# Kernel tuning notes

Hardware: AMD Instinct MI355X
Metric: run time of the kernel (lower is better)

Reference implementation:

```python
import jax, jax.numpy as jnp
import numpy as np


def gcn_conv(x, src, dst, deg_inv_sqrt, W, b):
    # PyG GCNConv: h = x @ W, then symmetric-normalized scatter-add over edges
    # (edge list already includes self-loops; deg computed over it).
    h = x @ W                                   # [N, F_out]
    norm = deg_inv_sqrt[src] * deg_inv_sqrt[dst]  # [E]
    msgs = h[src] * norm[:, None]               # gather + scale
    out = jax.ops.segment_sum(msgs, dst, num_segments=x.shape[0])
    return out + b


def setup_inputs() -> dict:
    key = jax.random.key(0)
    k1, k2, k3, k4 = jax.random.split(key, 4)
    N, E, F_in, F_hid, F_out = 200000, 6400000, 128, 8, 16
    x = jax.random.normal(k1, (N, F_in), dtype=jnp.float32)
    edge_index = jax.random.randint(k2, (2, E), 0, N, dtype=jnp.int64)
    W1 = jax.random.normal(k3, (F_in, F_hid), dtype=jnp.float32) * (1.0 / np.sqrt(F_in))
    b1 = jnp.zeros((F_hid,), dtype=jnp.float32)
    W2 = jax.random.normal(k4, (F_hid, F_out), dtype=jnp.float32) * (1.0 / np.sqrt(F_hid))
    b2 = jnp.zeros((F_out,), dtype=jnp.float32)
    return {"x": x, "edge_index": edge_index, "W1": W1, "b1": b1, "W2": W2, "b2": b2}


def reference(x, edge_index, W1, b1, W2, b2):
    N = x.shape[0]
    # add self-loops (GCNConv default add_self_loops=True)
    loops = jnp.arange(N, dtype=edge_index.dtype)
    src = jnp.concatenate([edge_index[0], loops])
    dst = jnp.concatenate([edge_index[1], loops])
    deg = jax.ops.segment_sum(jnp.ones_like(dst, dtype=x.dtype), dst, num_segments=N)
    deg_inv_sqrt = jnp.where(deg > 0, jax.lax.rsqrt(deg), 0.0)
    h = jax.nn.relu(gcn_conv(x, src, dst, deg_inv_sqrt, W1, b1))
    # dropout is identity in eval mode (training=False)
    out = gcn_conv(h, src, dst, deg_inv_sqrt, W2, b2)
    return out
```

## Files before the change

### kernel.cpp

```cpp
#include <hip/hip_runtime.h>
#include <hip/hip_fp16.h>

#define F_IN  128
#define F_HID 8
#define F_OUT 16

#define SBSH  9
#define SBW   (1 << SBSH)
#define MAXB  400
#define BIN_CAP  32
#define FLUSH_G  16


__global__ void init_gcur(int* __restrict__ gcur, int cap, int B) {
    int b = blockIdx.x * blockDim.x + threadIdx.x;
    if (b < B) gcur[b] = b * cap;
}

__global__ __launch_bounds__(512) void stage_bin(const int* __restrict__ ei,
                                                 int* __restrict__ gcur,
                                                 int* __restrict__ stage,
                                                 int E, int B, int per_block) {
    __shared__ int bin_cnt[MAXB];
    __shared__ int bin_buf[MAXB * BIN_CAP];
    for (int i = threadIdx.x; i < B; i += blockDim.x) bin_cnt[i] = 0;
    __syncthreads();
    const bool vec = ((E & 3) == 0);
    int base = blockIdx.x * per_block;
    int end  = min(E, base + per_block);
    for (int it = base; it < end; it += (int)blockDim.x * 4) {
        int e = it + (int)threadIdx.x * 4;
        int sv[4], dv[4], m4 = 0;
        if (vec && e + 3 < end) {
            int4 s4 = *(const int4*)(ei + e);
            int4 d4 = *(const int4*)(ei + E + e);
            sv[0] = s4.x; sv[1] = s4.y; sv[2] = s4.z; sv[3] = s4.w;
            dv[0] = d4.x; dv[1] = d4.y; dv[2] = d4.z; dv[3] = d4.w;
            m4 = 4;
        } else {
            for (int q = 0; e + q < end && q < 4; q++) { sv[q] = ei[e + q]; dv[q] = ei[E + e + q]; m4++; }
        }
        for (int q = 0; q < m4; q++) {
            int b   = dv[q] >> SBSH;
            int val = (sv[q] << SBSH) | (dv[q] & (SBW - 1));
            int pos = atomicAdd(&bin_cnt[b], 1);
            if (pos < BIN_CAP) {
                bin_buf[b * BIN_CAP + ((pos + b) & (BIN_CAP - 1))] = val;
            } else {
                int gp = atomicAdd(&gcur[b], 1);
                stage[gp] = val;
            }
        }
        __syncthreads();
        for (int b2 = threadIdx.x; b2 < B; b2 += blockDim.x) {
            int c = min(bin_cnt[b2], BIN_CAP);
            if (c >= FLUSH_G) {
                int m = c & ~(FLUSH_G - 1);
                int r = atomicAdd(&gcur[b2], m);
                for (int k = 0; k < m; k++)
                    stage[r + k] = bin_buf[b2 * BIN_CAP + ((k + b2) & (BIN_CAP - 1))];
                for (int k = m; k < c; k++)
                    bin_buf[b2 * BIN_CAP + ((k - m + b2) & (BIN_CAP - 1))] =
                        bin_buf[b2 * BIN_CAP + ((k + b2) & (BIN_CAP - 1))];
                bin_cnt[b2] = c - m;
            } else {
                bin_cnt[b2] = c;
            }
        }
        __syncthreads();
    }
    for (int b2 = threadIdx.x; b2 < B; b2 += blockDim.x) {
        int c = min(bin_cnt[b2], BIN_CAP);
        if (c > 0) {
            int r = atomicAdd(&gcur[b2], c);
            for (int k = 0; k < c; k++)
                stage[r + k] = bin_buf[b2 * BIN_CAP + ((k + b2) & (BIN_CAP - 1))];
        }
    }
}

__global__ __launch_bounds__(512) void scatter_csr(const int* __restrict__ stage,
                                                   const int* __restrict__ gcur,
                                                   int cap,
                                                   int* __restrict__ cnt,
                                                   float* __restrict__ dis,
                                                   int* __restrict__ row_start,
                                                   int* __restrict__ csr, int n) {
    __shared__ int s0[SBW], s1[SBW];
    int b  = blockIdx.x;
    int nb = b << SBSH;
    int i  = threadIdx.x;
    s0[i] = 0;
    __syncthreads();
    int base = b * cap;
    int num  = gcur[b] - base;
    for (int k = i; k < num; k += 512)
        atomicAdd(&s0[stage[base + k] & (SBW - 1)], 1);
    __syncthreads();
    int c = s0[i];
    if (nb + i < n) { cnt[nb + i] = c; dis[nb + i] = rsqrtf((float)(c + 1)); }
    int* src = s0; int* dst = s1;
    for (int off = 1; off < SBW; off <<= 1) {
        int v = src[i] + ((i >= off) ? src[i - off] : 0);
        dst[i] = v;
        __syncthreads();
        int* t = src; src = dst; dst = t;
    }
    int e = base + src[i] - c;
    if (nb + i < n) row_start[nb + i] = e;
    dst[i] = e;
    __syncthreads();
    for (int k = i; k < num; k += 512) {
        int v = stage[base + k];
        int pos = atomicAdd(&dst[v & (SBW - 1)], 1);
        csr[pos] = v >> SBSH;
    }
}

__global__ __launch_bounds__(256) void gemm1(const float* __restrict__ x,
                                             const float* __restrict__ W1,
                                             const float* __restrict__ dis,
                                             __half* __restrict__ g1, int n) {
    __shared__ float w[F_IN * F_HID];
    for (int i = threadIdx.x; i < F_IN * F_HID; i += blockDim.x) w[i] = W1[i];
    __syncthreads();
    int node = blockIdx.x * blockDim.x + threadIdx.x;
    if (node >= n) return;
    const float4* xr = (const float4*)(x + (size_t)node * F_IN);
    float acc[F_HID];
#pragma unroll
    for (int f = 0; f < F_HID; f++) acc[f] = 0.0f;
#pragma unroll
    for (int j = 0; j < F_IN / 4; j++) {
        float4 v = xr[j];
        const float* wr = &w[j * 4 * F_HID];
#pragma unroll
        for (int f = 0; f < F_HID; f++)
            acc[f] += v.x * wr[f] + v.y * wr[F_HID + f] + v.z * wr[2 * F_HID + f] + v.w * wr[3 * F_HID + f];
    }
    float d = dis[node];
    __half2 h[4];
#pragma unroll
    for (int p = 0; p < 4; p++) h[p] = __floats2half2_rn(acc[2 * p] * d, acc[2 * p + 1] * d);
    *(uint4*)(g1 + (size_t)node * F_HID) = *(uint4*)h;
}

__global__ __launch_bounds__(256) void aggregate_relu(const int* __restrict__ csr,
                                                      const int* __restrict__ row_start,
                                                      const int* __restrict__ cnt,
                                                      const float* __restrict__ dis,
                                                      const float* __restrict__ b1,
                                                      const __half* __restrict__ gin,
                                                      __half* __restrict__ gout, int n) {
    __shared__ float bb[F_HID];
    if (threadIdx.x < F_HID) bb[threadIdx.x] = b1[threadIdx.x];
    __syncthreads();
    int t = blockIdx.x * blockDim.x + threadIdx.x;
    int node = t >> 3;
    int f = t & 7;
    if (node >= n) return;
    int beg = row_start[node];
    int c   = cnt[node];
    float acc = __half2float(gin[(size_t)node * F_HID + f]);
    int j = 0;
    for (; j + 3 < c; j += 4) {
        int s0 = __builtin_nontemporal_load(csr + beg + j);
        int s1 = __builtin_nontemporal_load(csr + beg + j + 1);
        int s2 = __builtin_nontemporal_load(csr + beg + j + 2);
        int s3 = __builtin_nontemporal_load(csr + beg + j + 3);
        float a0 = __half2float(gin[(size_t)s0 * F_HID + f]);
        float a1 = __half2float(gin[(size_t)s1 * F_HID + f]);
        float a2 = __half2float(gin[(size_t)s2 * F_HID + f]);
        float a3 = __half2float(gin[(size_t)s3 * F_HID + f]);
        acc += (a0 + a1) + (a2 + a3);
    }
    for (; j < c; j++) {
        int s = __builtin_nontemporal_load(csr + beg + j);
        acc += __half2float(gin[(size_t)s * F_HID + f]);
    }
    float d = dis[node];
    float r = fmaxf(acc * d + bb[f], 0.0f) * d;
    gout[(size_t)node * F_HID + f] = __float2half(r);
}

__global__ __launch_bounds__(256) void aggregate_out(const int* __restrict__ csr,
                                                     const int* __restrict__ row_start,
                                                     const int* __restrict__ cnt,
                                                     const float* __restrict__ dis,
                                                     const float* __restrict__ W2,
                                                     const float* __restrict__ b2,
                                                     const __half* __restrict__ gin,
                                                     float* __restrict__ out, int n) {
    __shared__ float w[F_HID * F_OUT];
    __shared__ float bb[F_OUT];
    if (threadIdx.x < F_HID * F_OUT) w[threadIdx.x] = W2[threadIdx.x];
    if (threadIdx.x < F_OUT) bb[threadIdx.x] = b2[threadIdx.x];
    __syncthreads();
    int t = blockIdx.x * blockDim.x + threadIdx.x;
    int node = t >> 3;
    int f = t & 7;
    if (node >= n) return;
    int beg = row_start[node];
    int c   = cnt[node];
    float acc = __half2float(gin[(size_t)node * F_HID + f]);
    int j = 0;
    for (; j + 3 < c; j += 4) {
        int s0 = __builtin_nontemporal_load(csr + beg + j);
        int s1 = __builtin_nontemporal_load(csr + beg + j + 1);
        int s2 = __builtin_nontemporal_load(csr + beg + j + 2);
        int s3 = __builtin_nontemporal_load(csr + beg + j + 3);
        float a0 = __half2float(gin[(size_t)s0 * F_HID + f]);
        float a1 = __half2float(gin[(size_t)s1 * F_HID + f]);
        float a2 = __half2float(gin[(size_t)s2 * F_HID + f]);
        float a3 = __half2float(gin[(size_t)s3 * F_HID + f]);
        acc += (a0 + a1) + (a2 + a3);
    }
    for (; j < c; j++) {
        int s = __builtin_nontemporal_load(csr + beg + j);
        acc += __half2float(gin[(size_t)s * F_HID + f]);
    }
    float a_self = acc * dis[node];
    float o0 = bb[2 * f], o1 = bb[2 * f + 1];
#pragma unroll
    for (int k = 0; k < 8; k++) {
        float ak = __shfl(a_self, k, 8);
        o0 += ak * w[k * F_OUT + 2 * f];
        o1 += ak * w[k * F_OUT + 2 * f + 1];
    }
    *(float2*)(out + (size_t)node * F_OUT + 2 * f) = make_float2(o0, o1);
}

extern "C" void kernel_launch(void* const* d_in, const int* in_sizes, int n_in,
                              void* d_out, int out_size, void* d_ws, size_t ws_size,
                              hipStream_t stream) {
    const float* x  = (const float*)d_in[0];
    const int*   ei = (const int*)d_in[1];
    const float* W1 = (const float*)d_in[2];
    const float* b1 = (const float*)d_in[3];
    const float* W2 = (const float*)d_in[4];
    const float* b2 = (const float*)d_in[5];
    float* out = (float*)d_out;

    const int N = in_sizes[0] / F_IN;
    const int E = in_sizes[1] / 2;
    const int B = (N + SBW - 1) >> SBSH;

    int avg = (E + B - 1) / B;
    int cap = (avg + avg / 16 + 255) & ~255;

    int*    stage     = (int*)d_ws;
    int*    csr       = stage + (size_t)B * cap;
    float*  dis       = (float*)(csr + (size_t)B * cap);
    __half* gA        = (__half*)(dis + N);
    __half* gB        = (__half*)((int*)gA + (size_t)N * 4);
    int*    cnt       = (int*)gB + (size_t)N * 4;
    int*    row_start = cnt + N;
    int*    gcur      = row_start + N;

    const int BT = 256;
    dim3 blkN((N + BT - 1) / BT), thr(BT);
    dim3 blkA(((size_t)N * F_HID + BT - 1) / BT);

    int per_block = ((E + 639) / 640 + 2047) & ~2047;
    int SBLK = (E + per_block - 1) / per_block;

    init_gcur     <<<dim3((B + BT - 1) / BT), thr, 0, stream>>>(gcur, cap, B);
    stage_bin     <<<dim3(SBLK), dim3(512), 0, stream>>>(ei, gcur, stage, E, B, per_block);
    scatter_csr   <<<dim3(B),   dim3(512), 0, stream>>>(stage, gcur, cap, cnt, dis, row_start, csr, N);
    gemm1         <<<blkN, thr, 0, stream>>>(x, W1, dis, gA, N);
    aggregate_relu<<<blkA, thr, 0, stream>>>(csr, row_start, cnt, dis, b1, gA, gB, N);
    aggregate_out <<<blkA, thr, 0, stream>>>(csr, row_start, cnt, dis, W2, b2, gB, out, N);
}
```

Measured before the change: 464.6 us.

## Flush bins with whole wavefronts and aggregate features as half2 pairs

```diff
diff --git a/kernel.cpp b/kernel.cpp
--- a/kernel.cpp
+++ b/kernel.cpp
@@ -26,6 +26,8 @@
     for (int i = threadIdx.x; i < B; i += blockDim.x) bin_cnt[i] = 0;
     __syncthreads();
     const bool vec = ((E & 3) == 0);
+    const int wave = threadIdx.x >> 6;
+    const int lane = threadIdx.x & 63;
     int base = blockIdx.x * per_block;
     int end  = min(E, base + per_block);
     for (int it = base; it < end; it += (int)blockDim.x * 4) {
@@ -52,29 +54,34 @@
             }
         }
         __syncthreads();
-        for (int b2 = threadIdx.x; b2 < B; b2 += blockDim.x) {
+        for (int b2 = wave; b2 < B; b2 += 8) {
             int c = min(bin_cnt[b2], BIN_CAP);
             if (c >= FLUSH_G) {
                 int m = c & ~(FLUSH_G - 1);
-                int r = atomicAdd(&gcur[b2], m);
-                for (int k = 0; k < m; k++)
-                    stage[r + k] = bin_buf[b2 * BIN_CAP + ((k + b2) & (BIN_CAP - 1))];
-                for (int k = m; k < c; k++)
-                    bin_buf[b2 * BIN_CAP + ((k - m + b2) & (BIN_CAP - 1))] =
-                        bin_buf[b2 * BIN_CAP + ((k + b2) & (BIN_CAP - 1))];
-                bin_cnt[b2] = c - m;
-            } else {
+                int r = 0;
+                if (lane == 0) r = atomicAdd(&gcur[b2], m);
+                r = __shfl(r, 0);
+                if (lane < m)
+                    stage[r + lane] = bin_buf[b2 * BIN_CAP + ((lane + b2) & (BIN_CAP - 1))];
+                int rem = c - m;
+                int tmp = 0;
+                if (lane < rem) tmp = bin_buf[b2 * BIN_CAP + ((m + lane + b2) & (BIN_CAP - 1))];
+                if (lane < rem) bin_buf[b2 * BIN_CAP + ((lane + b2) & (BIN_CAP - 1))] = tmp;
+                if (lane == 0) bin_cnt[b2] = rem;
+            } else if (lane == 0) {
                 bin_cnt[b2] = c;
             }
         }
         __syncthreads();
     }
-    for (int b2 = threadIdx.x; b2 < B; b2 += blockDim.x) {
+    for (int b2 = wave; b2 < B; b2 += 8) {
         int c = min(bin_cnt[b2], BIN_CAP);
         if (c > 0) {
-            int r = atomicAdd(&gcur[b2], c);
-            for (int k = 0; k < c; k++)
-                stage[r + k] = bin_buf[b2 * BIN_CAP + ((k + b2) & (BIN_CAP - 1))];
+            int r = 0;
+            if (lane == 0) r = atomicAdd(&gcur[b2], c);
+            r = __shfl(r, 0);
+            if (lane < c)
+                stage[r + lane] = bin_buf[b2 * BIN_CAP + ((lane + b2) & (BIN_CAP - 1))];
         }
     }
 }
@@ -150,37 +157,40 @@
                                                       const int* __restrict__ cnt,
                                                       const float* __restrict__ dis,
                                                       const float* __restrict__ b1,
-                                                      const __half* __restrict__ gin,
-                                                      __half* __restrict__ gout, int n) {
+                                                      const __half2* __restrict__ gin,
+                                                      __half2* __restrict__ gout, int n) {
     __shared__ float bb[F_HID];
     if (threadIdx.x < F_HID) bb[threadIdx.x] = b1[threadIdx.x];
     __syncthreads();
     int t = blockIdx.x * blockDim.x + threadIdx.x;
-    int node = t >> 3;
-    int f = t & 7;
+    int node = t >> 2;
+    int f2 = t & 3;
     if (node >= n) return;
     int beg = row_start[node];
     int c   = cnt[node];
-    float acc = __half2float(gin[(size_t)node * F_HID + f]);
+    float2 acc = __half22float2(gin[(size_t)node * 4 + f2]);
     int j = 0;
     for (; j + 3 < c; j += 4) {
         int s0 = __builtin_nontemporal_load(csr + beg + j);
         int s1 = __builtin_nontemporal_load(csr + beg + j + 1);
         int s2 = __builtin_nontemporal_load(csr + beg + j + 2);
         int s3 = __builtin_nontemporal_load(csr + beg + j + 3);
-        float a0 = __half2float(gin[(size_t)s0 * F_HID + f]);
-        float a1 = __half2float(gin[(size_t)s1 * F_HID + f]);
-        float a2 = __half2float(gin[(size_t)s2 * F_HID + f]);
-        float a3 = __half2float(gin[(size_t)s3 * F_HID + f]);
-        acc += (a0 + a1) + (a2 + a3);
+        float2 a0 = __half22float2(gin[(size_t)s0 * 4 + f2]);
+        float2 a1 = __half22float2(gin[(size_t)s1 * 4 + f2]);
+        float2 a2 = __half22float2(gin[(size_t)s2 * 4 + f2]);
+        float2 a3 = __half22float2(gin[(size_t)s3 * 4 + f2]);
+        acc.x += (a0.x + a1.x) + (a2.x + a3.x);
+        acc.y += (a0.y + a1.y) + (a2.y + a3.y);
     }
     for (; j < c; j++) {
         int s = __builtin_nontemporal_load(csr + beg + j);
-        acc += __half2float(gin[(size_t)s * F_HID + f]);
+        float2 a = __half22float2(gin[(size_t)s * 4 + f2]);
+        acc.x += a.x; acc.y += a.y;
     }
     float d = dis[node];
-    float r = fmaxf(acc * d + bb[f], 0.0f) * d;
-    gout[(size_t)node * F_HID + f] = __float2half(r);
+    float r0 = fmaxf(acc.x * d + bb[2 * f2], 0.0f) * d;
+    float r1 = fmaxf(acc.y * d + bb[2 * f2 + 1], 0.0f) * d;
+    gout[(size_t)node * 4 + f2] = __floats2half2_rn(r0, r1);
 }
 
 __global__ __launch_bounds__(256) void aggregate_out(const int* __restrict__ csr,
@@ -189,7 +199,7 @@
                                                      const float* __restrict__ dis,
                                                      const float* __restrict__ W2,
                                                      const float* __restrict__ b2,
-                                                     const __half* __restrict__ gin,
+                                                     const __half2* __restrict__ gin,
                                                      float* __restrict__ out, int n) {
     __shared__ float w[F_HID * F_OUT];
     __shared__ float bb[F_OUT];
@@ -197,37 +207,41 @@
     if (threadIdx.x < F_OUT) bb[threadIdx.x] = b2[threadIdx.x];
     __syncthreads();
     int t = blockIdx.x * blockDim.x + threadIdx.x;
-    int node = t >> 3;
-    int f = t & 7;
+    int node = t >> 2;
+    int f2 = t & 3;
     if (node >= n) return;
     int beg = row_start[node];
     int c   = cnt[node];
-    float acc = __half2float(gin[(size_t)node * F_HID + f]);
+    float2 acc = __half22float2(gin[(size_t)node * 4 + f2]);
     int j = 0;
     for (; j + 3 < c; j += 4) {
         int s0 = __builtin_nontemporal_load(csr + beg + j);
         int s1 = __builtin_nontemporal_load(csr + beg + j + 1);
         int s2 = __builtin_nontemporal_load(csr + beg + j + 2);
         int s3 = __builtin_nontemporal_load(csr + beg + j + 3);
-        float a0 = __half2float(gin[(size_t)s0 * F_HID + f]);
-        float a1 = __half2float(gin[(size_t)s1 * F_HID + f]);
-        float a2 = __half2float(gin[(size_t)s2 * F_HID + f]);
-        float a3 = __half2float(gin[(size_t)s3 * F_HID + f]);
-        acc += (a0 + a1) + (a2 + a3);
+        float2 a0 = __half22float2(gin[(size_t)s0 * 4 + f2]);
+        float2 a1 = __half22float2(gin[(size_t)s1 * 4 + f2]);
+        float2 a2 = __half22float2(gin[(size_t)s2 * 4 + f2]);
+        float2 a3 = __half22float2(gin[(size_t)s3 * 4 + f2]);
+        acc.x += (a0.x + a1.x) + (a2.x + a3.x);
+        acc.y += (a0.y + a1.y) + (a2.y + a3.y);
     }
     for (; j < c; j++) {
         int s = __builtin_nontemporal_load(csr + beg + j);
-        acc += __half2float(gin[(size_t)s * F_HID + f]);
-    }
-    float a_self = acc * dis[node];
-    float o0 = bb[2 * f], o1 = bb[2 * f + 1];
+        float2 a = __half22float2(gin[(size_t)s * 4 + f2]);
+        acc.x += a.x; acc.y += a.y;
+    }
+    float d = dis[node];
+    float ax = acc.x * d, ay = acc.y * d;
+    int cbase = 4 * f2;
+    float o0 = bb[cbase], o1 = bb[cbase + 1], o2 = bb[cbase + 2], o3 = bb[cbase + 3];
 #pragma unroll
     for (int k = 0; k < 8; k++) {
-        float ak = __shfl(a_self, k, 8);
-        o0 += ak * w[k * F_OUT + 2 * f];
-        o1 += ak * w[k * F_OUT + 2 * f + 1];
-    }
-    *(float2*)(out + (size_t)node * F_OUT + 2 * f) = make_float2(o0, o1);
+        float ak = __shfl((k & 1) ? ay : ax, k >> 1, 4);
+        const float* wr = &w[k * F_OUT + cbase];
+        o0 += ak * wr[0]; o1 += ak * wr[1]; o2 += ak * wr[2]; o3 += ak * wr[3];
+    }
+    *(float4*)(out + (size_t)node * F_OUT + cbase) = make_float4(o0, o1, o2, o3);
 }
 
 extern "C" void kernel_launch(void* const* d_in, const int* in_sizes, int n_in,
@@ -248,18 +262,18 @@
     int avg = (E + B - 1) / B;
     int cap = (avg + avg / 16 + 255) & ~255;
 
-    int*    stage     = (int*)d_ws;
-    int*    csr       = stage + (size_t)B * cap;
-    float*  dis       = (float*)(csr + (size_t)B * cap);
-    __half* gA        = (__half*)(dis + N);
-    __half* gB        = (__half*)((int*)gA + (size_t)N * 4);
-    int*    cnt       = (int*)gB + (size_t)N * 4;
-    int*    row_start = cnt + N;
-    int*    gcur      = row_start + N;
+    int*     stage     = (int*)d_ws;
+    int*     csr       = stage + (size_t)B * cap;
+    float*   dis       = (float*)(csr + (size_t)B * cap);
+    __half2* gA        = (__half2*)(dis + N);
+    __half2* gB        = (__half2*)((int*)gA + (size_t)N * 4);
+    int*     cnt       = (int*)gB + (size_t)N * 4;
+    int*     row_start = cnt + N;
+    int*     gcur      = row_start + N;
 
     const int BT = 256;
     dim3 blkN((N + BT - 1) / BT), thr(BT);
-    dim3 blkA(((size_t)N * F_HID + BT - 1) / BT);
+    dim3 blkA(((size_t)N * 4 + BT - 1) / BT);
 
     int per_block = ((E + 639) / 640 + 2047) & ~2047;
     int SBLK = (E + per_block - 1) / per_block;
@@ -267,7 +281,7 @@
     init_gcur     <<<dim3((B + BT - 1) / BT), thr, 0, stream>>>(gcur, cap, B);
     stage_bin     <<<dim3(SBLK), dim3(512), 0, stream>>>(ei, gcur, stage, E, B, per_block);
     scatter_csr   <<<dim3(B),   dim3(512), 0, stream>>>(stage, gcur, cap, cnt, dis, row_start, csr, N);
-    gemm1         <<<blkN, thr, 0, stream>>>(x, W1, dis, gA, N);
+    gemm1         <<<blkN, thr, 0, stream>>>(x, W1, dis, (__half*)gA, N);
     aggregate_relu<<<blkA, thr, 0, stream>>>(csr, row_start, cnt, dis, b1, gA, gB, N);
     aggregate_out <<<blkA, thr, 0, stream>>>(csr, row_start, cnt, dis, W2, b2, gB, out, N);
 }
```

New measurement: 962.4 us. 2.07x slower.
